# Optimization experiments

Measured on AMD Instinct MI355X. Metric: run time of the kernel, lower is better.

The kernel has to match this reference:

```python
import jax, jax.numpy as jnp
import numpy as np

NEG_SLOPE = 0.2  # PyG GATConv default leaky_relu slope
EPS = 1e-16      # PyG softmax denominator epsilon


def gat_conv(x, src, dst, n_nodes, W, att_src, att_dst, bias, concat):
    # x: [N, Din]; W: [Din, H*F]; att_src/att_dst: [H, F]; bias: [H*F] or [F]
    H, F = att_src.shape
    h = (x @ W).reshape(n_nodes, H, F)                 # [N, H, F]
    a_src = jnp.einsum('nhf,hf->nh', h, att_src)       # [N, H]
    a_dst = jnp.einsum('nhf,hf->nh', h, att_dst)       # [N, H]
    e = jax.nn.leaky_relu(a_src[src] + a_dst[dst], NEG_SLOPE)  # [E, H]
    # segment softmax over incoming edges of each destination node
    m = jax.ops.segment_max(e, dst, num_segments=n_nodes)      # [N, H]
    ex = jnp.exp(e - m[dst])                                   # [E, H]
    s = jax.ops.segment_sum(ex, dst, num_segments=n_nodes)     # [N, H]
    alpha = ex / (s[dst] + EPS)                                # [E, H]
    msg = alpha[:, :, None] * h[src]                           # [E, H, F]
    out = jax.ops.segment_sum(msg, dst, num_segments=n_nodes)  # [N, H, F]
    if concat:
        out = out.reshape(n_nodes, H * F)
    else:
        out = out.mean(axis=1)
    return out + bias


def setup_inputs() -> dict:
    key = jax.random.key(0)
    ks = jax.random.split(key, 12)
    N, E, Din, Fh, H, C = 50000, 800000, 512, 32, 8, 40
    x = jax.random.normal(ks[0], (N, Din), dtype=jnp.float32)
    edge_index = jax.random.randint(ks[1], (2, E), 0, N, dtype=jnp.int64)
    g1 = 1.0 / np.sqrt(Din)
    g2 = 1.0 / np.sqrt(H * Fh)
    return {
        'x': x,
        'edge_index': edge_index,
        'W1': jax.random.normal(ks[2], (Din, H * Fh), dtype=jnp.float32) * g1,
        'att_src1': jax.random.normal(ks[3], (H, Fh), dtype=jnp.float32) * g2,
        'att_dst1': jax.random.normal(ks[4], (H, Fh), dtype=jnp.float32) * g2,
        'b1': jnp.zeros((H * Fh,), dtype=jnp.float32),
        'W2': jax.random.normal(ks[5], (H * Fh, C), dtype=jnp.float32) * g2,
        'att_src2': jax.random.normal(ks[6], (1, C), dtype=jnp.float32) * 0.1,
        'att_dst2': jax.random.normal(ks[7], (1, C), dtype=jnp.float32) * 0.1,
        'b2': jnp.zeros((C,), dtype=jnp.float32),
    }


def reference(x, edge_index, W1, att_src1, att_dst1, b1, W2, att_src2, att_dst2, b2):
    N = x.shape[0]
    # PyG GATConv adds self-loops by default
    loop = jnp.arange(N, dtype=edge_index.dtype)
    src = jnp.concatenate([edge_index[0], loop])
    dst = jnp.concatenate([edge_index[1], loop])
    # eval mode: dropout layers are identity
    h = gat_conv(x, src, dst, N, W1, att_src1, att_dst1, b1, concat=True)
    h = jax.nn.elu(h)
    out = gat_conv(h, src, dst, N, W2, att_src2, att_dst2, b2, concat=False)
    return jax.nn.log_softmax(out, axis=1)
```

## Files before the change

### kernel.cpp

```cpp
#include <hip/hip_runtime.h>
#include <hip/hip_bf16.h>
#include <math.h>

#define NN_DIN 512
#define NN_HF  256
#define NN_H   8
#define NN_F   32
#define NN_C   40

typedef short bf16x8 __attribute__((ext_vector_type(8)));
typedef float f32x4 __attribute__((ext_vector_type(4)));

__device__ __forceinline__ unsigned short f2bf_rne(float x) {
    unsigned u = __builtin_bit_cast(unsigned, x);
    unsigned r = u + 0x7FFFu + ((u >> 16) & 1u);
    return (unsigned short)(r >> 16);
}
__device__ __forceinline__ float bfu2f(unsigned short s) {
    unsigned u = ((unsigned)s) << 16;
    return __builtin_bit_cast(float, u);
}

__global__ __launch_bounds__(256) void w1rne_kernel(
    const float* __restrict__ W1, unsigned short* __restrict__ Wh)
{
    __shared__ float tile[32][33];
    int bk = blockIdx.x * 32;
    int bn = blockIdx.y * 32;
    int tx = threadIdx.x & 31, ty = threadIdx.x >> 5;
    #pragma unroll
    for (int i = 0; i < 32; i += 8)
        tile[ty + i][tx] = W1[(size_t)(bk + ty + i) * NN_HF + bn + tx];
    __syncthreads();
    #pragma unroll
    for (int i = 0; i < 32; i += 8) {
        float v = tile[tx][ty + i];
        Wh[(size_t)(bn + ty + i) * NN_DIN + bk + tx] = f2bf_rne(v);
    }
}

#define G1_BM 128
#define G1_BN 64
#define G1_BK 64
#define G1_LDK 72

__global__ __launch_bounds__(256) void gemm1_kernel(
    const float* __restrict__ A, const unsigned short* __restrict__ BT,
    unsigned short* __restrict__ Cb, int M)
{
    __shared__ unsigned short Ah[G1_BM][G1_LDK];
    __shared__ unsigned short Bh[G1_BN][G1_LDK];
    const int m0 = blockIdx.x * G1_BM;
    const int n0 = blockIdx.y * G1_BN;
    const int tid = threadIdx.x;
    const int wave = tid >> 6, lane = tid & 63;
    const int wm = wave >> 1, wn = wave & 1;
    const int lr = lane & 15, lg = lane >> 4;

    const int amr[8] = { (tid + 0*256) >> 4, (tid + 1*256) >> 4, (tid + 2*256) >> 4,
                         (tid + 3*256) >> 4, (tid + 4*256) >> 4, (tid + 5*256) >> 4,
                         (tid + 6*256) >> 4, (tid + 7*256) >> 4 };
    const int akc = (tid & 15) << 2;
    const int bnr0 = tid >> 3, bnr1 = (tid + 256) >> 3;
    const int bkc = (tid & 7) << 3;

    f32x4 acc[4][2];
    #pragma unroll
    for (int i = 0; i < 4; ++i)
        #pragma unroll
        for (int j = 0; j < 2; ++j) acc[i][j] = (f32x4){0.f, 0.f, 0.f, 0.f};

    float4 ra[8];
    bf16x8 rb[2];

    #pragma unroll
    for (int i = 0; i < 8; ++i) {
        ra[i] = make_float4(0.f, 0.f, 0.f, 0.f);
        if (m0 + amr[i] < M)
            ra[i] = *(const float4*)(A + (size_t)(m0 + amr[i]) * NN_DIN + akc);
    }
    rb[0] = *(const bf16x8*)(BT + (size_t)(n0 + bnr0) * NN_DIN + bkc);
    rb[1] = *(const bf16x8*)(BT + (size_t)(n0 + bnr1) * NN_DIN + bkc);
    #pragma unroll
    for (int i = 0; i < 8; ++i) {
        ushort4 hv;
        hv.x = f2bf_rne(ra[i].x); hv.y = f2bf_rne(ra[i].y);
        hv.z = f2bf_rne(ra[i].z); hv.w = f2bf_rne(ra[i].w);
        *reinterpret_cast<ushort4*>(&Ah[amr[i]][akc]) = hv;
    }
    *reinterpret_cast<bf16x8*>(&Bh[bnr0][bkc]) = rb[0];
    *reinterpret_cast<bf16x8*>(&Bh[bnr1][bkc]) = rb[1];
    __syncthreads();

    const int NSTEP = NN_DIN / G1_BK;
    for (int step = 0; step < NSTEP; ++step) {
        const bool last = (step == NSTEP - 1);
        if (!last) {
            int k0 = (step + 1) * G1_BK;
            #pragma unroll
            for (int i = 0; i < 8; ++i) {
                ra[i] = make_float4(0.f, 0.f, 0.f, 0.f);
                if (m0 + amr[i] < M)
                    ra[i] = *(const float4*)(A + (size_t)(m0 + amr[i]) * NN_DIN + k0 + akc);
            }
            rb[0] = *(const bf16x8*)(BT + (size_t)(n0 + bnr0) * NN_DIN + k0 + bkc);
            rb[1] = *(const bf16x8*)(BT + (size_t)(n0 + bnr1) * NN_DIN + k0 + bkc);
        }
        #pragma unroll
        for (int ks = 0; ks < 2; ++ks) {
            const int kb = (ks << 5) + (lg << 3);
            bf16x8 fah[4], fbh[2];
            #pragma unroll
            for (int mi = 0; mi < 4; ++mi) {
                int m = (wm << 6) + (mi << 4) + lr;
                fah[mi] = *reinterpret_cast<const bf16x8*>(&Ah[m][kb]);
            }
            #pragma unroll
            for (int ni = 0; ni < 2; ++ni) {
                int n = (wn << 5) + (ni << 4) + lr;
                fbh[ni] = *reinterpret_cast<const bf16x8*>(&Bh[n][kb]);
            }
            #pragma unroll
            for (int mi = 0; mi < 4; ++mi)
                #pragma unroll
                for (int ni = 0; ni < 2; ++ni)
                    acc[mi][ni] = __builtin_amdgcn_mfma_f32_16x16x32_bf16(
                        fah[mi], fbh[ni], acc[mi][ni], 0, 0, 0);
        }
        __syncthreads();
        if (!last) {
            #pragma unroll
            for (int i = 0; i < 8; ++i) {
                ushort4 hv;
                hv.x = f2bf_rne(ra[i].x); hv.y = f2bf_rne(ra[i].y);
                hv.z = f2bf_rne(ra[i].z); hv.w = f2bf_rne(ra[i].w);
                *reinterpret_cast<ushort4*>(&Ah[amr[i]][akc]) = hv;
            }
            *reinterpret_cast<bf16x8*>(&Bh[bnr0][bkc]) = rb[0];
            *reinterpret_cast<bf16x8*>(&Bh[bnr1][bkc]) = rb[1];
            __syncthreads();
        }
    }
    #pragma unroll
    for (int mi = 0; mi < 4; ++mi)
        #pragma unroll
        for (int ni = 0; ni < 2; ++ni)
            #pragma unroll
            for (int r = 0; r < 4; ++r) {
                int row = m0 + (wm << 6) + (mi << 4) + (lg << 2) + r;
                int col = n0 + (wn << 5) + (ni << 4) + lr;
                if (row < M)
                    Cb[(size_t)row * NN_HF + col] = f2bf_rne(acc[mi][ni][r]);
            }
}

__global__ __launch_bounds__(256) void attn1_kernel(
    const unsigned short* __restrict__ h1b, const float* __restrict__ att_s,
    const float* __restrict__ att_d, float* __restrict__ a1s,
    float* __restrict__ a1d)
{
    int n = blockIdx.x;
    int t = threadIdx.x;
    float hv = bfu2f(h1b[(size_t)n * NN_HF + t]);
    float ps = hv * att_s[t];
    float pd = hv * att_d[t];
    #pragma unroll
    for (int off = 16; off >= 1; off >>= 1) {
        ps += __shfl_down(ps, off, 32);
        pd += __shfl_down(pd, off, 32);
    }
    if ((t & 31) == 0) {
        a1s[n * NN_H + (t >> 5)] = ps;
        a1d[n * NN_H + (t >> 5)] = pd;
    }
}

__global__ void count_kernel(const int* __restrict__ dst, int* __restrict__ deg,
                             int E, int Nn)
{
    int e = blockIdx.x * blockDim.x + threadIdx.x;
    int Et = E + Nn;
    if (e >= Et) return;
    int d = (e < E) ? dst[e] : (e - E);
    atomicAdd(&deg[d], 1);
}

#define SCAN_CHUNK 1024
__global__ __launch_bounds__(256) void scan1_kernel(
    const int* __restrict__ deg, int* __restrict__ offs,
    int* __restrict__ bsums, int Nn)
{
    __shared__ int sh[256];
    int b = blockIdx.x, t = threadIdx.x;
    int base = b * SCAN_CHUNK + t * 4;
    int v[4];
    int tot = 0;
    #pragma unroll
    for (int i = 0; i < 4; ++i) {
        v[i] = (base + i < Nn) ? deg[base + i] : 0;
        tot += v[i];
    }
    sh[t] = tot;
    __syncthreads();
    for (int off = 1; off < 256; off <<= 1) {
        int y = (t >= off) ? sh[t - off] : 0;
        __syncthreads();
        sh[t] += y;
        __syncthreads();
    }
    int p = sh[t] - tot;
    #pragma unroll
    for (int i = 0; i < 4; ++i) {
        if (base + i < Nn) offs[base + i] = p;
        p += v[i];
    }
    if (t == 255) bsums[b] = sh[255];
}

__global__ void scan2_kernel(int* __restrict__ bsums, int nb)
{
    if (threadIdx.x == 0) {
        int run = 0;
        for (int i = 0; i < nb; ++i) {
            int tmp = bsums[i];
            bsums[i] = run;
            run += tmp;
        }
    }
}

__global__ void scan3_kernel(int* __restrict__ offs, const int* __restrict__ bsums,
                             int Nn, int Et)
{
    int i = blockIdx.x * blockDim.x + threadIdx.x;
    if (i < Nn) offs[i] += bsums[i >> 10];
    if (i == 0) offs[Nn] = Et;
}

__global__ void fill_kernel(const int* __restrict__ src, const int* __restrict__ dst,
                            const int* __restrict__ offs, int* __restrict__ cursor,
                            int* __restrict__ srcs, int E, int Nn)
{
    int e = blockIdx.x * blockDim.x + threadIdx.x;
    int Et = E + Nn;
    if (e >= Et) return;
    int d, s;
    if (e < E) { d = dst[e]; s = src[e]; }
    else       { d = e - E;  s = e - E;  }
    int pos = offs[d] + atomicAdd(&cursor[d], 1);
    srcs[pos] = s;
}

__global__ __launch_bounds__(256) void attw1_kernel(
    const float* __restrict__ a1s, const float* __restrict__ a1d,
    const int* __restrict__ offs, const int* __restrict__ srcs,
    float* __restrict__ alpha1, int Nn)
{
    int n = blockIdx.x * 4 + (threadIdx.x >> 6);
    if (n >= Nn) return;
    int lane = threadIdx.x & 63;
    int g = lane >> 3, h = lane & 7;
    int beg = offs[n], end = offs[n + 1];
    float adn = a1d[n * NN_H + h];
    float m = -3.0e38f, s = 0.f;
    for (int k = beg + g; k < end; k += 8) {
        int sN = srcs[k];
        float e = a1s[sN * NN_H + h] + adn;
        e = e > 0.f ? e : 0.2f * e;
        float nm = fmaxf(m, e);
        float sc = __expf(m - nm);
        s = s * sc + __expf(e - nm);
        m = nm;
    }
    #pragma unroll
    for (int off = 8; off < 64; off <<= 1) {
        float mo = __shfl_xor(m, off);
        float so = __shfl_xor(s, off);
        float nm = fmaxf(m, mo);
        s = s * __expf(m - nm) + so * __expf(mo - nm);
        m = nm;
    }
    float inv = 1.f / (s + 1e-16f);
    for (int k = beg + g; k < end; k += 8) {
        int sN = srcs[k];
        float e = a1s[sN * NN_H + h] + adn;
        e = e > 0.f ? e : 0.2f * e;
        alpha1[(size_t)k * NN_H + h] = __expf(e - m) * inv;
    }
}

__global__ __launch_bounds__(256) void agg1_kernel(
    const unsigned short* __restrict__ h1b, const float* __restrict__ alpha1,
    const int* __restrict__ offs, const int* __restrict__ srcs,
    const float* __restrict__ b1, unsigned short* __restrict__ hp1b, int Nn)
{
    int n = blockIdx.x * 4 + (threadIdx.x >> 6);
    if (n >= Nn) return;
    int lane = threadIdx.x & 63;
    int h = lane >> 3;
    int beg = offs[n], end = offs[n + 1];
    f32x4 a0 = {0.f,0.f,0.f,0.f}, a1 = a0, a2 = a0, a3 = a0;
    int k = beg;
    for (; k + 3 < end; k += 4) {
        int s0 = srcs[k], s1 = srcs[k+1], s2 = srcs[k+2], s3 = srcs[k+3];
        float w0 = alpha1[(size_t)k * NN_H + h];
        float w1 = alpha1[(size_t)(k+1) * NN_H + h];
        float w2 = alpha1[(size_t)(k+2) * NN_H + h];
        float w3 = alpha1[(size_t)(k+3) * NN_H + h];
        ushort4 v0 = *(const ushort4*)(h1b + (size_t)s0 * NN_HF + lane * 4);
        ushort4 v1 = *(const ushort4*)(h1b + (size_t)s1 * NN_HF + lane * 4);
        ushort4 v2 = *(const ushort4*)(h1b + (size_t)s2 * NN_HF + lane * 4);
        ushort4 v3 = *(const ushort4*)(h1b + (size_t)s3 * NN_HF + lane * 4);
        a0.x = fmaf(w0, bfu2f(v0.x), a0.x); a0.y = fmaf(w0, bfu2f(v0.y), a0.y);
        a0.z = fmaf(w0, bfu2f(v0.z), a0.z); a0.w = fmaf(w0, bfu2f(v0.w), a0.w);
        a1.x = fmaf(w1, bfu2f(v1.x), a1.x); a1.y = fmaf(w1, bfu2f(v1.y), a1.y);
        a1.z = fmaf(w1, bfu2f(v1.z), a1.z); a1.w = fmaf(w1, bfu2f(v1.w), a1.w);
        a2.x = fmaf(w2, bfu2f(v2.x), a2.x); a2.y = fmaf(w2, bfu2f(v2.y), a2.y);
        a2.z = fmaf(w2, bfu2f(v2.z), a2.z); a2.w = fmaf(w2, bfu2f(v2.w), a2.w);
        a3.x = fmaf(w3, bfu2f(v3.x), a3.x); a3.y = fmaf(w3, bfu2f(v3.y), a3.y);
        a3.z = fmaf(w3, bfu2f(v3.z), a3.z); a3.w = fmaf(w3, bfu2f(v3.w), a3.w);
    }
    for (; k < end; ++k) {
        int s0 = srcs[k];
        float w0 = alpha1[(size_t)k * NN_H + h];
        ushort4 v0 = *(const ushort4*)(h1b + (size_t)s0 * NN_HF + lane * 4);
        a0.x = fmaf(w0, bfu2f(v0.x), a0.x); a0.y = fmaf(w0, bfu2f(v0.y), a0.y);
        a0.z = fmaf(w0, bfu2f(v0.z), a0.z); a0.w = fmaf(w0, bfu2f(v0.w), a0.w);
    }
    f32x4 acc;
    acc[0] = (a0.x + a1.x) + (a2.x + a3.x);
    acc[1] = (a0.y + a1.y) + (a2.y + a3.y);
    acc[2] = (a0.z + a1.z) + (a2.z + a3.z);
    acc[3] = (a0.w + a1.w) + (a2.w + a3.w);
    float4 bb = *(const float4*)(b1 + lane * 4);
    float r0 = acc[0] + bb.x, r1 = acc[1] + bb.y;
    float r2 = acc[2] + bb.z, r3 = acc[3] + bb.w;
    r0 = r0 > 0.f ? r0 : __expf(r0) - 1.f;
    r1 = r1 > 0.f ? r1 : __expf(r1) - 1.f;
    r2 = r2 > 0.f ? r2 : __expf(r2) - 1.f;
    r3 = r3 > 0.f ? r3 : __expf(r3) - 1.f;
    ushort4 o = make_ushort4(f2bf_rne(r0), f2bf_rne(r1), f2bf_rne(r2), f2bf_rne(r3));
    *(ushort4*)(hp1b + (size_t)n * NN_HF + lane * 4) = o;
}

#define G2_ROWS 64
#define G2_KC   64

__global__ __launch_bounds__(256) void gemm2_kernel(
    const unsigned short* __restrict__ Ab, const float* __restrict__ W2,
    const float* __restrict__ att_s, const float* __restrict__ att_d,
    float* __restrict__ h2, float* __restrict__ a2s, float* __restrict__ a2d,
    int M)
{
    __shared__ float As[G2_ROWS][G2_KC + 1];
    __shared__ float Ws[G2_KC][NN_C];
    int m0 = blockIdx.x * G2_ROWS;
    int t = threadIdx.x;
    int rp = t >> 3;
    int cg = t & 7;
    int c0 = cg * 5;
    int r0 = rp * 2, r1 = r0 + 1;
    float acc[2][5] = {};
    for (int kc = 0; kc < NN_HF; kc += G2_KC) {
        #pragma unroll
        for (int i = 0; i < 4; ++i) {
            int g = t + i * 256;
            int r = g >> 4;
            int k4 = (g & 15) << 2;
            ushort4 v = make_ushort4(0, 0, 0, 0);
            if (m0 + r < M)
                v = *(const ushort4*)(Ab + (size_t)(m0 + r) * NN_HF + kc + k4);
            As[r][k4 + 0] = bfu2f(v.x); As[r][k4 + 1] = bfu2f(v.y);
            As[r][k4 + 2] = bfu2f(v.z); As[r][k4 + 3] = bfu2f(v.w);
        }
        #pragma unroll
        for (int i = 0; i < 10; ++i) {
            int g = t + i * 256;
            int k = g / NN_C, c = g % NN_C;
            Ws[k][c] = W2[(size_t)(kc + k) * NN_C + c];
        }
        __syncthreads();
        #pragma unroll 4
        for (int k = 0; k < G2_KC; ++k) {
            float a0 = As[r0][k];
            float a1 = As[r1][k];
            #pragma unroll
            for (int j = 0; j < 5; ++j) {
                float w = Ws[k][c0 + j];
                acc[0][j] += a0 * w;
                acc[1][j] += a1 * w;
            }
        }
        __syncthreads();
    }
    #pragma unroll
    for (int i = 0; i < 2; ++i) {
        int m = m0 + r0 + i;
        float ps = 0.f, pd = 0.f;
        #pragma unroll
        for (int j = 0; j < 5; ++j) {
            float v = acc[i][j];
            ps += v * att_s[c0 + j];
            pd += v * att_d[c0 + j];
            if (m < M) h2[(size_t)m * NN_C + c0 + j] = v;
        }
        #pragma unroll
        for (int off = 4; off >= 1; off >>= 1) {
            ps += __shfl_down(ps, off, 8);
            pd += __shfl_down(pd, off, 8);
        }
        if (cg == 0 && m < M) { a2s[m] = ps; a2d[m] = pd; }
    }
}

__global__ __launch_bounds__(256) void attw2_kernel(
    const float* __restrict__ a2s, const float* __restrict__ a2d,
    const int* __restrict__ offs, const int* __restrict__ srcs,
    float* __restrict__ alpha2, int Nn)
{
    int n = blockIdx.x * 4 + (threadIdx.x >> 6);
    if (n >= Nn) return;
    int lane = threadIdx.x & 63;
    int beg = offs[n], end = offs[n + 1];
    float adn = a2d[n];
    float m = -3.0e38f, s = 0.f;
    for (int k = beg + lane; k < end; k += 64) {
        int sN = srcs[k];
        float e = a2s[sN] + adn;
        e = e > 0.f ? e : 0.2f * e;
        float nm = fmaxf(m, e);
        float sc = __expf(m - nm);
        s = s * sc + __expf(e - nm);
        m = nm;
    }
    #pragma unroll
    for (int off = 1; off < 64; off <<= 1) {
        float mo = __shfl_xor(m, off);
        float so = __shfl_xor(s, off);
        float nm = fmaxf(m, mo);
        s = s * __expf(m - nm) + so * __expf(mo - nm);
        m = nm;
    }
    float inv = 1.f / (s + 1e-16f);
    for (int k = beg + lane; k < end; k += 64) {
        int sN = srcs[k];
        float e = a2s[sN] + adn;
        e = e > 0.f ? e : 0.2f * e;
        alpha2[k] = __expf(e - m) * inv;
    }
}

__global__ __launch_bounds__(256) void agg2_kernel(
    const float* __restrict__ h2, const float* __restrict__ alpha2,
    const int* __restrict__ offs, const int* __restrict__ srcs,
    const float* __restrict__ b2, float* __restrict__ out, int Nn)
{
    int n = blockIdx.x * 4 + (threadIdx.x >> 6);
    if (n >= Nn) return;
    int f = threadIdx.x & 63;
    int beg = offs[n], end = offs[n + 1];
    float a0 = 0.f, a1 = 0.f, a2 = 0.f, a3 = 0.f;
    int k = beg;
    for (; k + 3 < end; k += 4) {
        int s0 = srcs[k], s1 = srcs[k+1], s2 = srcs[k+2], s3 = srcs[k+3];
        float w0 = alpha2[k], w1 = alpha2[k+1], w2 = alpha2[k+2], w3 = alpha2[k+3];
        float h0 = (f < NN_C) ? h2[(size_t)s0 * NN_C + f] : 0.f;
        float h1 = (f < NN_C) ? h2[(size_t)s1 * NN_C + f] : 0.f;
        float h2v = (f < NN_C) ? h2[(size_t)s2 * NN_C + f] : 0.f;
        float h3 = (f < NN_C) ? h2[(size_t)s3 * NN_C + f] : 0.f;
        a0 = fmaf(w0, h0, a0); a1 = fmaf(w1, h1, a1);
        a2 = fmaf(w2, h2v, a2); a3 = fmaf(w3, h3, a3);
    }
    for (; k < end; ++k) {
        int s0 = srcs[k];
        float w0 = alpha2[k];
        float h0 = (f < NN_C) ? h2[(size_t)s0 * NN_C + f] : 0.f;
        a0 = fmaf(w0, h0, a0);
    }
    float acc = (a0 + a1) + (a2 + a3);
    float v = acc + ((f < NN_C) ? b2[f] : 0.f);
    float lg = (f < NN_C) ? v : -INFINITY;
    float mx = lg;
    #pragma unroll
    for (int off = 32; off >= 1; off >>= 1) mx = fmaxf(mx, __shfl_xor(mx, off));
    float w2e = (f < NN_C) ? __expf(lg - mx) : 0.f;
    float sum = w2e;
    #pragma unroll
    for (int off = 32; off >= 1; off >>= 1) sum += __shfl_xor(sum, off);
    if (f < NN_C) out[(size_t)n * NN_C + f] = lg - mx - __logf(sum);
}

extern "C" void kernel_launch(void* const* d_in, const int* in_sizes, int n_in,
                              void* d_out, int out_size, void* d_ws, size_t ws_size,
                              hipStream_t stream)
{
    const float* x    = (const float*)d_in[0];
    const int*   ei   = (const int*)d_in[1];
    const float* W1   = (const float*)d_in[2];
    const float* as1  = (const float*)d_in[3];
    const float* ad1  = (const float*)d_in[4];
    const float* b1   = (const float*)d_in[5];
    const float* W2   = (const float*)d_in[6];
    const float* as2  = (const float*)d_in[7];
    const float* ad2  = (const float*)d_in[8];
    const float* b2   = (const float*)d_in[9];
    float* out = (float*)d_out;

    int Nn = in_sizes[0] / NN_DIN;
    int E  = in_sizes[1] / 2;
    int Et = E + Nn;
    const int* srcIdx = ei;
    const int* dstIdx = ei + E;

    char* ws = (char*)d_ws;
    size_t off = 0;
    auto alloc = [&](size_t bytes) {
        void* p = ws + off;
        off = (off + bytes + 255) & ~(size_t)255;
        return p;
    };
    unsigned short* h1b  = (unsigned short*)alloc((size_t)Nn * NN_HF * 2);
    unsigned short* W1T  = (unsigned short*)alloc((size_t)NN_HF * NN_DIN * 2);
    unsigned short* hp1b = (unsigned short*)alloc((size_t)Nn * NN_HF * 2);
    float* a1s  = (float*)alloc((size_t)Nn * NN_H * 4);
    float* a1d  = (float*)alloc((size_t)Nn * NN_H * 4);
    float* h2   = (float*)alloc((size_t)Nn * NN_C * 4);
    float* a2s  = (float*)alloc((size_t)Nn * 4);
    float* a2d  = (float*)alloc((size_t)Nn * 4);
    float* alpha1 = (float*)alloc((size_t)Et * NN_H * 4);
    float* alpha2 = (float*)alloc((size_t)Et * 4);
    int*   deg  = (int*)alloc((size_t)Nn * 4);
    int*   offs = (int*)alloc((size_t)(Nn + 1) * 4);
    int*   bsums= (int*)alloc(1024 * 4);
    int*   curs = (int*)alloc((size_t)Nn * 4);
    int*   srcs = (int*)alloc((size_t)Et * 4);

    hipMemsetAsync(deg, 0, (size_t)Nn * 4, stream);
    hipMemsetAsync(curs, 0, (size_t)Nn * 4, stream);

    w1rne_kernel<<<dim3(NN_DIN / 32, NN_HF / 32), 256, 0, stream>>>(W1, W1T);

    dim3 g1((Nn + G1_BM - 1) / G1_BM, NN_HF / G1_BN);
    gemm1_kernel<<<g1, 256, 0, stream>>>(x, W1T, h1b, Nn);

    attn1_kernel<<<Nn, 256, 0, stream>>>(h1b, as1, ad1, a1s, a1d);

    count_kernel<<<(Et + 255) / 256, 256, 0, stream>>>(dstIdx, deg, E, Nn);
    int nb = (Nn + SCAN_CHUNK - 1) / SCAN_CHUNK;
    scan1_kernel<<<nb, 256, 0, stream>>>(deg, offs, bsums, Nn);
    scan2_kernel<<<1, 64, 0, stream>>>(bsums, nb);
    scan3_kernel<<<(Nn + 255) / 256, 256, 0, stream>>>(offs, bsums, Nn, Et);
    fill_kernel<<<(Et + 255) / 256, 256, 0, stream>>>(srcIdx, dstIdx, offs, curs, srcs, E, Nn);

    attw1_kernel<<<(Nn + 3) / 4, 256, 0, stream>>>(a1s, a1d, offs, srcs, alpha1, Nn);
    agg1_kernel<<<(Nn + 3) / 4, 256, 0, stream>>>(h1b, alpha1, offs, srcs, b1, hp1b, Nn);

    gemm2_kernel<<<(Nn + G2_ROWS - 1) / G2_ROWS, 256, 0, stream>>>(
        hp1b, W2, as2, ad2, h2, a2s, a2d, Nn);

    attw2_kernel<<<(Nn + 3) / 4, 256, 0, stream>>>(a2s, a2d, offs, srcs, alpha2, Nn);
    agg2_kernel<<<(Nn + 3) / 4, 256, 0, stream>>>(h2, alpha2, offs, srcs, b2, out, Nn);
}
```

Before: 516.8 us.

## Retile first GEMM so each block covers the full output width

The first-layer GEMM block tile changes from 128x64 to 64x256, so each block computes every output column for its rows and the grid becomes one-dimensional. Each row of x (fp32, the dominant input) is then read from global memory and converted to bf16 once, instead of once per column tile. In exchange each block reloads the whole bf16 W1 (256x64 per k-step), the accumulator count per thread doubles, and shared memory per block grows, which may reduce occupancy.

```diff
diff --git a/kernel.cpp b/kernel.cpp
--- a/kernel.cpp
+++ b/kernel.cpp
@@ -39,8 +39,8 @@
     }
 }
 
-#define G1_BM 128
-#define G1_BN 64
+#define G1_BM 64
+#define G1_BN 256
 #define G1_BK 64
 #define G1_LDK 72
 
@@ -51,45 +51,48 @@
     __shared__ unsigned short Ah[G1_BM][G1_LDK];
     __shared__ unsigned short Bh[G1_BN][G1_LDK];
     const int m0 = blockIdx.x * G1_BM;
-    const int n0 = blockIdx.y * G1_BN;
     const int tid = threadIdx.x;
     const int wave = tid >> 6, lane = tid & 63;
-    const int wm = wave >> 1, wn = wave & 1;
+    const int wn = wave;
     const int lr = lane & 15, lg = lane >> 4;
 
-    const int amr[8] = { (tid + 0*256) >> 4, (tid + 1*256) >> 4, (tid + 2*256) >> 4,
-                         (tid + 3*256) >> 4, (tid + 4*256) >> 4, (tid + 5*256) >> 4,
-                         (tid + 6*256) >> 4, (tid + 7*256) >> 4 };
+    const int amr[4] = { (tid + 0*256) >> 4, (tid + 1*256) >> 4,
+                         (tid + 2*256) >> 4, (tid + 3*256) >> 4 };
     const int akc = (tid & 15) << 2;
-    const int bnr0 = tid >> 3, bnr1 = (tid + 256) >> 3;
+    const int bnr[8] = { (tid + 0*256) >> 3, (tid + 1*256) >> 3,
+                         (tid + 2*256) >> 3, (tid + 3*256) >> 3,
+                         (tid + 4*256) >> 3, (tid + 5*256) >> 3,
+                         (tid + 6*256) >> 3, (tid + 7*256) >> 3 };
     const int bkc = (tid & 7) << 3;
 
-    f32x4 acc[4][2];
+    f32x4 acc[4][4];
     #pragma unroll
     for (int i = 0; i < 4; ++i)
         #pragma unroll
-        for (int j = 0; j < 2; ++j) acc[i][j] = (f32x4){0.f, 0.f, 0.f, 0.f};
-
-    float4 ra[8];
-    bf16x8 rb[2];
-
-    #pragma unroll
-    for (int i = 0; i < 8; ++i) {
+        for (int j = 0; j < 4; ++j) acc[i][j] = (f32x4){0.f, 0.f, 0.f, 0.f};
+
+    float4 ra[4];
+    bf16x8 rb[8];
+
+    #pragma unroll
+    for (int i = 0; i < 4; ++i) {
         ra[i] = make_float4(0.f, 0.f, 0.f, 0.f);
         if (m0 + amr[i] < M)
             ra[i] = *(const float4*)(A + (size_t)(m0 + amr[i]) * NN_DIN + akc);
     }
-    rb[0] = *(const bf16x8*)(BT + (size_t)(n0 + bnr0) * NN_DIN + bkc);
-    rb[1] = *(const bf16x8*)(BT + (size_t)(n0 + bnr1) * NN_DIN + bkc);
-    #pragma unroll
-    for (int i = 0; i < 8; ++i) {
+    #pragma unroll
+    for (int i = 0; i < 8; ++i)
+        rb[i] = *(const bf16x8*)(BT + (size_t)bnr[i] * NN_DIN + bkc);
+    #pragma unroll
+    for (int i = 0; i < 4; ++i) {
         ushort4 hv;
         hv.x = f2bf_rne(ra[i].x); hv.y = f2bf_rne(ra[i].y);
         hv.z = f2bf_rne(ra[i].z); hv.w = f2bf_rne(ra[i].w);
         *reinterpret_cast<ushort4*>(&Ah[amr[i]][akc]) = hv;
     }
-    *reinterpret_cast<bf16x8*>(&Bh[bnr0][bkc]) = rb[0];
-    *reinterpret_cast<bf16x8*>(&Bh[bnr1][bkc]) = rb[1];
+    #pragma unroll
+    for (int i = 0; i < 8; ++i)
+        *reinterpret_cast<bf16x8*>(&Bh[bnr[i]][bkc]) = rb[i];
     __syncthreads();
 
     const int NSTEP = NN_DIN / G1_BK;
@@ -98,57 +101,59 @@
         if (!last) {
             int k0 = (step + 1) * G1_BK;
             #pragma unroll
-            for (int i = 0; i < 8; ++i) {
+            for (int i = 0; i < 4; ++i) {
                 ra[i] = make_float4(0.f, 0.f, 0.f, 0.f);
                 if (m0 + amr[i] < M)
                     ra[i] = *(const float4*)(A + (size_t)(m0 + amr[i]) * NN_DIN + k0 + akc);
             }
-            rb[0] = *(const bf16x8*)(BT + (size_t)(n0 + bnr0) * NN_DIN + k0 + bkc);
-            rb[1] = *(const bf16x8*)(BT + (size_t)(n0 + bnr1) * NN_DIN + k0 + bkc);
+            #pragma unroll
+            for (int i = 0; i < 8; ++i)
+                rb[i] = *(const bf16x8*)(BT + (size_t)bnr[i] * NN_DIN + k0 + bkc);
         }
         #pragma unroll
         for (int ks = 0; ks < 2; ++ks) {
             const int kb = (ks << 5) + (lg << 3);
-            bf16x8 fah[4], fbh[2];
+            bf16x8 fah[4], fbh[4];
             #pragma unroll
             for (int mi = 0; mi < 4; ++mi) {
-                int m = (wm << 6) + (mi << 4) + lr;
+                int m = (mi << 4) + lr;
                 fah[mi] = *reinterpret_cast<const bf16x8*>(&Ah[m][kb]);
             }
             #pragma unroll
-            for (int ni = 0; ni < 2; ++ni) {
-                int n = (wn << 5) + (ni << 4) + lr;
+            for (int ni = 0; ni < 4; ++ni) {
+                int n = (wn << 6) + (ni << 4) + lr;
                 fbh[ni] = *reinterpret_cast<const bf16x8*>(&Bh[n][kb]);
             }
             #pragma unroll
             for (int mi = 0; mi < 4; ++mi)
                 #pragma unroll
-                for (int ni = 0; ni < 2; ++ni)
+                for (int ni = 0; ni < 4; ++ni)
                     acc[mi][ni] = __builtin_amdgcn_mfma_f32_16x16x32_bf16(
                         fah[mi], fbh[ni], acc[mi][ni], 0, 0, 0);
         }
         __syncthreads();
         if (!last) {
             #pragma unroll
-            for (int i = 0; i < 8; ++i) {
+            for (int i = 0; i < 4; ++i) {
                 ushort4 hv;
                 hv.x = f2bf_rne(ra[i].x); hv.y = f2bf_rne(ra[i].y);
                 hv.z = f2bf_rne(ra[i].z); hv.w = f2bf_rne(ra[i].w);
                 *reinterpret_cast<ushort4*>(&Ah[amr[i]][akc]) = hv;
             }
-            *reinterpret_cast<bf16x8*>(&Bh[bnr0][bkc]) = rb[0];
-            *reinterpret_cast<bf16x8*>(&Bh[bnr1][bkc]) = rb[1];
+            #pragma unroll
+            for (int i = 0; i < 8; ++i)
+                *reinterpret_cast<bf16x8*>(&Bh[bnr[i]][bkc]) = rb[i];
             __syncthreads();
         }
     }
     #pragma unroll
     for (int mi = 0; mi < 4; ++mi)
         #pragma unroll
-        for (int ni = 0; ni < 2; ++ni)
+        for (int ni = 0; ni < 4; ++ni)
             #pragma unroll
             for (int r = 0; r < 4; ++r) {
-                int row = m0 + (wm << 6) + (mi << 4) + (lg << 2) + r;
-                int col = n0 + (wn << 5) + (ni << 4) + lr;
+                int row = m0 + (mi << 4) + (lg << 2) + r;
+                int col = (wn << 6) + (ni << 4) + lr;
                 if (row < M)
                     Cb[(size_t)row * NN_HF + col] = f2bf_rne(acc[mi][ni][r]);
             }
@@ -540,8 +545,7 @@
 
     w1rne_kernel<<<dim3(NN_DIN / 32, NN_HF / 32), 256, 0, stream>>>(W1, W1T);
 
-    dim3 g1((Nn + G1_BM - 1) / G1_BM, NN_HF / G1_BN);
-    gemm1_kernel<<<g1, 256, 0, stream>>>(x, W1T, h1b, Nn);
+    gemm1_kernel<<<(Nn + G1_BM - 1) / G1_BM, 256, 0, stream>>>(x, W1T, h1b, Nn);
 
     attn1_kernel<<<Nn, 256, 0, stream>>>(h1b, as1, ad1, a1s, a1d);
 
```

Result: faster. 494.3 us (-4.4%).
